# Kernel tuning notes

Hardware: AMD Instinct MI355X
Metric: run time of the kernel (lower is better)

Reference implementation:

```python
import jax, jax.numpy as jnp
import numpy as np

CHANNELS = 32
HIDDEN = 1024
LAYERS = 8
NODE_TYPES = 7
N_NODES = 500_000
N_EDGES = 2_000_000
NUM_GRAPHS = 1024


def setup_inputs() -> dict:
    key = jax.random.key(0)
    ks = jax.random.split(key, 8)
    nodes = jax.random.randint(ks[0], (N_NODES,), 0, NODE_TYPES)
    sources = jax.random.randint(ks[1], (N_EDGES,), 0, N_NODES)
    targets = jax.random.randint(ks[2], (N_EDGES,), 0, N_NODES)
    # sorted graph ids covering all NUM_GRAPHS graphs (no empty graphs)
    batch = (jnp.arange(N_NODES) * NUM_GRAPHS) // N_NODES
    emb = jax.random.normal(ks[3], (NODE_TYPES, CHANNELS), dtype=jnp.float32)
    # xavier-normal-ish init for the 8 layers x {out, back} 32x32 convs
    xavier_std = (2.0 / (CHANNELS + CHANNELS)) ** 0.5
    conv_w = jax.random.normal(ks[4], (LAYERS, 2, CHANNELS, CHANNELS), dtype=jnp.float32) * xavier_std
    hidden_w = jax.random.normal(ks[5], (CHANNELS, HIDDEN), dtype=jnp.float32) * 0.05
    hidden_b = jax.random.normal(ks[6], (HIDDEN,), dtype=jnp.float32) * 0.05
    out_w = jax.random.normal(ks[7], (HIDDEN, 1), dtype=jnp.float32) * 0.05
    return dict(nodes=nodes, sources=sources, targets=targets, batch=batch,
                emb=emb, conv_w=conv_w, hidden_w=hidden_w, hidden_b=hidden_b,
                out_w=out_w)


def reference(nodes, sources, targets, batch, emb, conv_w, hidden_w, hidden_b, out_w):
    n = nodes.shape[0]
    ones_e = jnp.ones(sources.shape[0], dtype=jnp.float32)
    # norm = 1 / (1 + in-degree), norm_t = 1 / (1 + out-degree)  [N,1]
    norm = (1.0 / (1.0 + jax.ops.segment_sum(ones_e, targets, num_segments=n)))[:, None]
    norm_t = (1.0 / (1.0 + jax.ops.segment_sum(ones_e, sources, num_segments=n)))[:, None]
    node_counts = jax.ops.segment_sum(jnp.ones(n, dtype=jnp.float32), batch,
                                      num_segments=NUM_GRAPHS)

    x = emb[nodes]  # [N, C]

    def conv(x, s, t, nrm, w):
        # x.index_add(0, t, x[s]) -> x + scatter_add of gathered source feats
        agg = nrm * (x + jax.ops.segment_sum(x[s], t, num_segments=n))
        return jax.nn.relu(agg @ w)

    for l in range(LAYERS):
        x = x + conv(x, sources, targets, norm, conv_w[l, 0]) \
              + conv(x, targets, sources, norm_t, conv_w[l, 1])

    # mean pooling per graph
    g = jax.ops.segment_sum(x, batch, num_segments=NUM_GRAPHS) / node_counts[:, None]
    h = jax.nn.relu(g @ hidden_w + hidden_b)
    return (h @ out_w).squeeze(-1)  # [NUM_GRAPHS]
```

## Files before the change

### kernel.cpp

```cpp
#include <hip/hip_runtime.h>

#define CHANNELS 32
#define HIDDEN 1024
#define LAYERS 8
#define NRANGE 8

typedef __attribute__((ext_vector_type(8))) short short8;
typedef __attribute__((ext_vector_type(4))) float float4v;

__device__ __forceinline__ short f2bf_rne(float f) {
    union { float f; unsigned u; } v; v.f = f;
    unsigned r = v.u + 0x7fffu + ((v.u >> 16) & 1u);
    return (short)(r >> 16);
}
__device__ __forceinline__ float bf2f(short h) {
    union { float f; unsigned u; } v; v.u = ((unsigned)(unsigned short)h) << 16;
    return v.f;
}
__device__ __forceinline__ float bfu2f(unsigned short h) {
    union { float f; unsigned u; } v; v.u = ((unsigned)h) << 16;
    return v.f;
}
__device__ __forceinline__ float bflo(unsigned u) {
    union { float f; unsigned u; } v; v.u = u << 16; return v.f;
}
__device__ __forceinline__ float bfhi(unsigned u) {
    union { float f; unsigned u; } v; v.u = u & 0xffff0000u; return v.f;
}
__device__ __forceinline__ unsigned packbf(float x, float y) {
    return ((unsigned)(unsigned short)f2bf_rne(y) << 16) |
            (unsigned)(unsigned short)f2bf_rne(x);
}


__global__ __launch_bounds__(256)
void pre_kernel(const int* __restrict__ src, const int* __restrict__ tgt,
                int* __restrict__ deg2,
                const int* __restrict__ nodes, const float* __restrict__ emb,
                unsigned short* __restrict__ hi0, unsigned short* __restrict__ lo,
                const int* __restrict__ batch, float* __restrict__ counts,
                int n_nodes, int n_edges, int n_graphs, int rsh,
                int degB, int initB) {
    int bid = blockIdx.x;
    int tid = threadIdx.x;
    if (bid < degB) {
        int r = bid & (NRANGE - 1);
        int chunk = bid >> 3;
        int base = chunk * 2048;
#pragma unroll
        for (int j = 0; j < 8; j++) {
            int e = base + j * 256 + tid;
            if (e < n_edges) {
                int t = __builtin_nontemporal_load(tgt + e);
                int s = __builtin_nontemporal_load(src + e);
                if ((t >> rsh) == r) atomicAdd(&deg2[t], 1);
                if ((s >> rsh) == r) atomicAdd(&deg2[n_nodes + s], 1);
            }
        }
    } else if (bid < degB + initB) {
        int gid = (bid - degB) * 256 + tid;
        int i = gid >> 2, c8 = (gid & 3) * 8;
        if (i < n_nodes) {
            const float* e = emb + nodes[i] * CHANNELS + c8;
            short8 hv, lv;
#pragma unroll
            for (int k = 0; k < 8; k++) {
                float v = e[k];
                short hsh = f2bf_rne(v);
                hv[k] = hsh;
                lv[k] = f2bf_rne(v - bf2f(hsh));
            }
            *(short8*)(hi0 + (size_t)i * CHANNELS + c8) = hv;
            *(short8*)(lo  + (size_t)i * CHANNELS + c8) = lv;
        }
    } else {
        int b = (bid - degB - initB) * 256 + tid;
        if (b < n_graphs) {
            int lo_i = 0, hi_i = n_nodes;
            while (lo_i < hi_i) { int mid = (lo_i + hi_i) >> 1; if (batch[mid] < b) lo_i = mid + 1; else hi_i = mid; }
            int s0 = lo_i;
            lo_i = 0; hi_i = n_nodes;
            while (lo_i < hi_i) { int mid = (lo_i + hi_i) >> 1; if (batch[mid] < b + 1) lo_i = mid + 1; else hi_i = mid; }
            counts[b] = (float)(lo_i - s0);
        }
    }
}


__global__ __launch_bounds__(256)
void scan_pass1(const int* __restrict__ deg, int* __restrict__ bs, int n) {
    __shared__ int sh[256];
    int t = threadIdx.x;
    int base = blockIdx.x * 2048 + t * 8;
    int s = 0;
#pragma unroll
    for (int j = 0; j < 8; j++) { int idx = base + j; if (idx < n) s += deg[idx]; }
    sh[t] = s; __syncthreads();
    for (int st = 128; st > 0; st >>= 1) { if (t < st) sh[t] += sh[t + st]; __syncthreads(); }
    if (t == 0) bs[blockIdx.x] = sh[0];
}

__global__ void scan_pass2(int* __restrict__ bs, int nb) {
    __shared__ int sh[1024];
    int t = threadIdx.x;
    int v = (t < nb) ? bs[t] : 0;
    sh[t] = v; __syncthreads();
    for (int off = 1; off < 1024; off <<= 1) {
        int u = (t >= off) ? sh[t - off] : 0; __syncthreads();
        sh[t] += u; __syncthreads();
    }
    if (t < nb) bs[t] = sh[t] - v;
}

__global__ __launch_bounds__(256)
void scan_pass3(const int* __restrict__ deg, const int* __restrict__ bs,
                int* __restrict__ off, int* __restrict__ cur, int n) {
    __shared__ int sh[256];
    int t = threadIdx.x;
    int base = blockIdx.x * 2048 + t * 8;
    int v[8]; int s = 0;
#pragma unroll
    for (int j = 0; j < 8; j++) { int idx = base + j; v[j] = (idx < n) ? deg[idx] : 0; s += v[j]; }
    sh[t] = s; __syncthreads();
    for (int st = 1; st < 256; st <<= 1) {
        int u = (t >= st) ? sh[t - st] : 0; __syncthreads();
        sh[t] += u; __syncthreads();
    }
    int acc = bs[blockIdx.x] + sh[t] - s;
#pragma unroll
    for (int j = 0; j < 8; j++) {
        int idx = base + j;
        if (idx < n) { off[idx] = acc; cur[idx] = acc; }
        acc += v[j];
    }
}


__global__ __launch_bounds__(256)
void scatter_range_kernel(const int* __restrict__ src, const int* __restrict__ tgt,
                          int* __restrict__ cur2, int* __restrict__ nbr,
                          int n_nodes, int n_edges, int rsh) {
    int r = blockIdx.x & 15;
    int chunk = blockIdx.x >> 4;
    int base = chunk * 2048;
#pragma unroll
    for (int j = 0; j < 8; j++) {
        int e = base + j * 256 + threadIdx.x;
        if (e < n_edges) {
            int t = __builtin_nontemporal_load(tgt + e);
            int s = __builtin_nontemporal_load(src + e);
            if ((t >> rsh) == r) { int p = atomicAdd(&cur2[t], 1);           nbr[p] = s; }
            if ((s >> rsh) == r) { int q = atomicAdd(&cur2[n_nodes + s], 1); nbr[q] = t; }
        }
    }
}


__global__ __launch_bounds__(256, 8)
void layer_mfma(const int* __restrict__ off2, const int* __restrict__ nbr,
                const float* __restrict__ wbase,
                const unsigned short* __restrict__ hi_in,
                unsigned short* __restrict__ hi_out,
                unsigned short* __restrict__ lo,
                int n_nodes, int n_edges) {
    __shared__ short A1h[64][32], A2h[64][32];
    __shared__ short W0h[32][32], W1h[32][32];
    __shared__ int offIn[65], offOut[65];

    int tid = threadIdx.x;
    int nodeblock = blockIdx.x * 64;

    const unsigned* hid = (const unsigned*)hi_in;
    const unsigned* lod = (const unsigned*)lo;

    for (int idx = tid; idx < CHANNELS * CHANNELS; idx += 256) {
        int k = idx >> 5, n = idx & 31;
        W0h[n][k] = f2bf_rne(wbase[idx]);
        W1h[n][k] = f2bf_rne(wbase[CHANNELS * CHANNELS + idx]);
    }
    if (tid < 65) {
        int idx = nodeblock + tid;
        offIn[tid]  = (idx <= n_nodes) ? off2[idx] : n_edges;
        int idx2 = n_nodes + idx;
        offOut[tid] = (idx2 < 2 * n_nodes) ? off2[idx2] : 2 * n_edges;
    }
    __syncthreads();

    int c = tid & 31, g = tid >> 5;
    int h = c >> 4;
    int cc = c & 15;

    int bi_c, d1_c, bo_c, d2_c, nbl1_c, nbl2_c, node_c;
    float xvx_c, xvy_c;
    {
        int local = g;
        node_c = nodeblock + local;
        bi_c = offIn[local];  d1_c = offIn[local + 1] - bi_c;
        bo_c = offOut[local]; d2_c = offOut[local + 1] - bo_c;
        nbl1_c = (c < d1_c) ? nbr[bi_c + c] : 0;
        nbl2_c = (c < d2_c) ? nbr[bo_c + c] : 0;
        xvx_c = 0.f; xvy_c = 0.f;
        if (node_c < n_nodes) {
            unsigned hp = hid[(unsigned)(node_c * 16 + cc)];
            unsigned lp = lod[(unsigned)(node_c * 16 + cc)];
            xvx_c = bflo(hp) + bflo(lp);
            xvy_c = bfhi(hp) + bfhi(lp);
        }
    }

#define GATHER8(B) { \
    int p0 = __shfl(nbl1_c, (B) + h,     32); \
    int p1 = __shfl(nbl1_c, (B) + 2 + h, 32); \
    int p2 = __shfl(nbl1_c, (B) + 4 + h, 32); \
    int p3 = __shfl(nbl1_c, (B) + 6 + h, 32); \
    int q0 = __shfl(nbl2_c, (B) + h,     32); \
    int q1 = __shfl(nbl2_c, (B) + 2 + h, 32); \
    int q2 = __shfl(nbl2_c, (B) + 4 + h, 32); \
    int q3 = __shfl(nbl2_c, (B) + 6 + h, 32); \
    bool a0 = (B) + h     < m1, a1 = (B) + 2 + h < m1; \
    bool a2 = (B) + 4 + h < m1, a3 = (B) + 6 + h < m1; \
    bool e0 = (B) + h     < m2, e1 = (B) + 2 + h < m2; \
    bool e2 = (B) + 4 + h < m2, e3 = (B) + 6 + h < m2; \
    p0 = a0 ? p0 : self; p1 = a1 ? p1 : self; \
    p2 = a2 ? p2 : self; p3 = a3 ? p3 : self; \
    q0 = e0 ? q0 : self; q1 = e1 ? q1 : self; \
    q2 = e2 ? q2 : self; q3 = e3 ? q3 : self; \
    unsigned u0 = hid[(unsigned)(p0 * 16 + cc)]; \
    unsigned u1 = hid[(unsigned)(p1 * 16 + cc)]; \
    unsigned u2 = hid[(unsigned)(p2 * 16 + cc)]; \
    unsigned u3 = hid[(unsigned)(p3 * 16 + cc)]; \
    unsigned w0 = hid[(unsigned)(q0 * 16 + cc)]; \
    unsigned w1 = hid[(unsigned)(q1 * 16 + cc)]; \
    unsigned w2 = hid[(unsigned)(q2 * 16 + cc)]; \
    unsigned w3 = hid[(unsigned)(q3 * 16 + cc)]; \
    s1x += a0 ? bflo(u0) : 0.f; s1y += a0 ? bfhi(u0) : 0.f; \
    s1x += a1 ? bflo(u1) : 0.f; s1y += a1 ? bfhi(u1) : 0.f; \
    s1x += a2 ? bflo(u2) : 0.f; s1y += a2 ? bfhi(u2) : 0.f; \
    s1x += a3 ? bflo(u3) : 0.f; s1y += a3 ? bfhi(u3) : 0.f; \
    s2x += e0 ? bflo(w0) : 0.f; s2y += e0 ? bfhi(w0) : 0.f; \
    s2x += e1 ? bflo(w1) : 0.f; s2y += e1 ? bfhi(w1) : 0.f; \
    s2x += e2 ? bflo(w2) : 0.f; s2y += e2 ? bfhi(w2) : 0.f; \
    s2x += e3 ? bflo(w3) : 0.f; s2y += e3 ? bfhi(w3) : 0.f; \
}

    for (int pass = 0; pass < 8; pass++) {
        int bi_n = 0, d1_n = 0, bo_n = 0, d2_n = 0, nbl1_n = 0, nbl2_n = 0, node_n = 0;
        float xvx_n = 0.f, xvy_n = 0.f;
        if (pass < 7) {
            int local = (pass + 1) * 8 + g;
            node_n = nodeblock + local;
            bi_n = offIn[local];  d1_n = offIn[local + 1] - bi_n;
            bo_n = offOut[local]; d2_n = offOut[local + 1] - bo_n;
            nbl1_n = (c < d1_n) ? nbr[bi_n + c] : 0;
            nbl2_n = (c < d2_n) ? nbr[bo_n + c] : 0;
            if (node_n < n_nodes) {
                unsigned hp = hid[(unsigned)(node_n * 16 + cc)];
                unsigned lp = lod[(unsigned)(node_n * 16 + cc)];
                xvx_n = bflo(hp) + bflo(lp);
                xvy_n = bfhi(hp) + bfhi(lp);
            }
        }

        int local = pass * 8 + g;
        int i = node_c;
        int self = (i < n_nodes) ? i : 0;

        int m1 = d1_c < 32 ? d1_c : 32;
        int m2 = d2_c < 32 ? d2_c : 32;
        int mm = m1 > m2 ? m1 : m2;

        float s1x = 0.f, s1y = 0.f, s2x = 0.f, s2y = 0.f;
        GATHER8(0)
        if (mm > 8)  GATHER8(8)
        if (mm > 16) GATHER8(16)
        if (mm > 24) GATHER8(24)

        s1x += __shfl_xor(s1x, 16, 32);
        s1y += __shfl_xor(s1y, 16, 32);
        s2x += __shfl_xor(s2x, 16, 32);
        s2y += __shfl_xor(s2y, 16, 32);

        for (int e = bi_c + 32; e < bi_c + d1_c; e++) {
            unsigned u = hid[(unsigned)(nbr[e] * 16 + cc)];
            s1x += bflo(u); s1y += bfhi(u);
        }
        for (int e = bo_c + 32; e < bo_c + d2_c; e++) {
            unsigned u = hid[(unsigned)(nbr[e] * 16 + cc)];
            s2x += bflo(u); s2y += bfhi(u);
        }

        unsigned pk1 = 0, pk2 = 0;
        if (i < n_nodes) {
            float n1 = 1.0f / (1.0f + (float)d1_c);
            float n2 = 1.0f / (1.0f + (float)d2_c);
            pk1 = packbf(n1 * (xvx_c + s1x), n1 * (xvy_c + s1y));
            pk2 = packbf(n2 * (xvx_c + s2x), n2 * (xvy_c + s2y));
        }
        unsigned* dst = (h == 0) ? (unsigned*)&A1h[local][2 * cc]
                                 : (unsigned*)&A2h[local][2 * cc];
        *dst = (h == 0) ? pk1 : pk2;

        bi_c = bi_n; d1_c = d1_n; bo_c = bo_n; d2_c = d2_n;
        nbl1_c = nbl1_n; nbl2_c = nbl2_n;
        xvx_c = xvx_n; xvy_c = xvy_n; node_c = node_n;
    }
#undef GATHER8
    __syncthreads();

    int wv = tid >> 6, lane = tid & 63;
    int m = lane & 15, quad = lane >> 4;
    int row0 = wv * 16;

    short8 a1h = *(const short8*)&A1h[row0 + m][quad * 8];
    short8 a2h = *(const short8*)&A2h[row0 + m][quad * 8];

    float4v dd[4];
#pragma unroll
    for (int hh = 0; hh < 2; hh++) {
        int n0 = hh * 16 + m;
        short8 b0h = *(const short8*)&W0h[n0][quad * 8];
        short8 b1h = *(const short8*)&W1h[n0][quad * 8];
        float4v d1 = {0.f, 0.f, 0.f, 0.f};
        d1 = __builtin_amdgcn_mfma_f32_16x16x32_bf16(a1h, b0h, d1, 0, 0, 0);
        float4v d2 = {0.f, 0.f, 0.f, 0.f};
        d2 = __builtin_amdgcn_mfma_f32_16x16x32_bf16(a2h, b1h, d2, 0, 0, 0);
        dd[hh * 2] = d1; dd[hh * 2 + 1] = d2;
    }

#pragma unroll
    for (int hh = 0; hh < 2; hh++) {
        float4v d1 = dd[hh * 2], d2 = dd[hh * 2 + 1];
#pragma unroll
        for (int r = 0; r < 4; r++) {
            int local = row0 + quad * 4 + r;
            int node = nodeblock + local;
            if (node < n_nodes) {
                int col = hh * 16 + m;
                size_t idx = (size_t)node * CHANNELS + col;
                float base = bfu2f(hi_in[idx]) + bfu2f(lo[idx]);
                float v = base + fmaxf(d1[r], 0.f) + fmaxf(d2[r], 0.f);
                short hn = f2bf_rne(v);
                hi_out[idx] = (unsigned short)hn;
                lo[idx]     = (unsigned short)f2bf_rne(v - bf2f(hn));
            }
        }
    }
}


#define POOL_CHUNK 1024

__global__ __launch_bounds__(256)
void pool_kernel(const int* __restrict__ batch,
                 const unsigned short* __restrict__ hi,
                 const unsigned short* __restrict__ lo,
                 float* __restrict__ g, int n_nodes) {
    int c = threadIdx.x & 31;
    int r = threadIdx.x >> 5;
    int base = blockIdx.x * POOL_CHUNK;
    float acc = 0.f;
    int cur = -1;
    for (int it = 0; it < POOL_CHUNK / 8; it++) {
        int node = base + it * 8 + r;
        if (node >= n_nodes) break;
        int b = batch[node];
        if (b != cur) {
            if (cur >= 0) atomicAdd(&g[cur * CHANNELS + c], acc);
            acc = 0.f;
            cur = b;
        }
        size_t idx = (size_t)node * CHANNELS + c;
        acc += bfu2f(hi[idx]) + bfu2f(lo[idx]);
    }
    if (cur >= 0) atomicAdd(&g[cur * CHANNELS + c], acc);
}


__global__ __launch_bounds__(256)
void mlp_kernel(const float* __restrict__ g, const float* __restrict__ counts,
                const float* __restrict__ hidden_w, const float* __restrict__ hidden_b,
                const float* __restrict__ out_w, float* __restrict__ out) {
    __shared__ float grow[CHANNELS];
    __shared__ float red[256];
    int graph = blockIdx.x;
    int tid = threadIdx.x;
    if (tid < CHANNELS) grow[tid] = g[graph * CHANNELS + tid] / counts[graph];
    __syncthreads();
    float partial = 0.f;
    for (int q = 0; q < HIDDEN / 256; q++) {
        int j = q * 256 + tid;
        float h = hidden_b[j];
#pragma unroll
        for (int k = 0; k < CHANNELS; k++) h += grow[k] * hidden_w[k * HIDDEN + j];
        partial += fmaxf(h, 0.f) * out_w[j];
    }
    red[tid] = partial;
    __syncthreads();
    for (int s = 128; s > 0; s >>= 1) {
        if (tid < s) red[tid] += red[tid + s];
        __syncthreads();
    }
    if (tid == 0) out[graph] = red[0];
}


extern "C" void kernel_launch(void* const* d_in, const int* in_sizes, int n_in,
                              void* d_out, int out_size, void* d_ws, size_t ws_size,
                              hipStream_t stream) {
    const int*   nodes    = (const int*)d_in[0];
    const int*   sources  = (const int*)d_in[1];
    const int*   targets  = (const int*)d_in[2];
    const int*   batch    = (const int*)d_in[3];
    const float* emb      = (const float*)d_in[4];
    const float* conv_w   = (const float*)d_in[5];
    const float* hidden_w = (const float*)d_in[6];
    const float* hidden_b = (const float*)d_in[7];
    const float* out_w    = (const float*)d_in[8];
    float* out = (float*)d_out;

    const int n_nodes  = in_sizes[0];
    const int n_edges  = in_sizes[1];
    const int n_graphs = out_size;
    const int n2 = 2 * n_nodes;

    int rsh8 = 0;
    while (((n_nodes - 1) >> rsh8) >= 8) rsh8++;
    int rsh16 = 0;
    while (((n_nodes - 1) >> rsh16) >= 16) rsh16++;

    char* ws = (char*)d_ws;
    unsigned short* hi0 = (unsigned short*)ws; ws += (size_t)n_nodes * CHANNELS * 2;
    unsigned short* hi1 = (unsigned short*)ws; ws += (size_t)n_nodes * CHANNELS * 2;
    unsigned short* lo  = (unsigned short*)ws; ws += (size_t)n_nodes * CHANNELS * 2;
    int*   deg2   = (int*)ws;   ws += (size_t)n2 * 4;
    int*   off2   = (int*)ws;   ws += (size_t)n2 * 4;
    int*   cur2   = (int*)ws;   ws += (size_t)n2 * 4;
    int*   nbr    = (int*)ws;   ws += (size_t)2 * n_edges * 4;
    int*   bsums  = (int*)ws;   ws += 4096;
    float* g      = (float*)ws; ws += (size_t)n_graphs * CHANNELS * 4;
    float* counts = (float*)ws; ws += (size_t)n_graphs * 4;

    hipMemsetAsync(deg2, 0, (size_t)n2 * 4, stream);
    hipMemsetAsync(g, 0, (size_t)n_graphs * CHANNELS * 4, stream);

    int echunks = (n_edges + 2047) / 2048;
    int degB  = echunks * NRANGE;
    int initB = (n_nodes * 4 + 255) / 256;
    int cntB  = (n_graphs + 255) / 256;

    pre_kernel<<<degB + initB + cntB, 256, 0, stream>>>(sources, targets, deg2,
                                                        nodes, emb, hi0, lo,
                                                        batch, counts,
                                                        n_nodes, n_edges, n_graphs,
                                                        rsh8, degB, initB);

    int nblk = (n2 + 2047) / 2048;
    scan_pass1<<<nblk, 256, 0, stream>>>(deg2, bsums, n2);
    scan_pass2<<<1, 1024, 0, stream>>>(bsums, nblk);
    scan_pass3<<<nblk, 256, 0, stream>>>(deg2, bsums, off2, cur2, n2);

    scatter_range_kernel<<<echunks * 16, 256, 0, stream>>>(sources, targets, cur2, nbr,
                                                           n_nodes, n_edges, rsh16);

    unsigned short* hin = hi0; unsigned short* hout = hi1;
    int lblocks = (n_nodes + 63) / 64;
    for (int l = 0; l < LAYERS; l++) {
        const float* wbase = conv_w + (size_t)l * 2 * CHANNELS * CHANNELS;
        layer_mfma<<<lblocks, 256, 0, stream>>>(off2, nbr, wbase,
                                                hin, hout, lo, n_nodes, n_edges);
        unsigned short* tmp = hin; hin = hout; hout = tmp;
    }

    int pool_blocks = (n_nodes + POOL_CHUNK - 1) / POOL_CHUNK;
    pool_kernel<<<pool_blocks, 256, 0, stream>>>(batch, hin, lo, g, n_nodes);
    mlp_kernel<<<n_graphs, 256, 0, stream>>>(g, counts, hidden_w, hidden_b, out_w, out);
}
```

Measured before the change: 1.560 ms.

## Cache self features in LDS, split gather granularity, adjust launch bounds and pool chunk

Stores each node's reconstructed fp32 self feature in a shared-memory tile during the gather phase, so the epilogue no longer re-reads hi/lo from global memory. The first neighbour gather batch is split into two 4-wide steps so low-degree nodes issue fewer loads. Launch bounds drop from 8 to 4 blocks per SM, and the pooling chunk size doubles. The extra 8 KB of LDS plus the looser occupancy hint may lower resident waves for a latency-bound gather kernel.

```diff
diff --git a/kernel.cpp b/kernel.cpp
--- a/kernel.cpp
+++ b/kernel.cpp
@@ -156,7 +156,7 @@
 }
 
 
-__global__ __launch_bounds__(256, 8)
+__global__ __launch_bounds__(256, 4)
 void layer_mfma(const int* __restrict__ off2, const int* __restrict__ nbr,
                 const float* __restrict__ wbase,
                 const unsigned short* __restrict__ hi_in,
@@ -165,6 +165,7 @@
                 int n_nodes, int n_edges) {
     __shared__ short A1h[64][32], A2h[64][32];
     __shared__ short W0h[32][32], W1h[32][32];
+    __shared__ float Xf[64][32];
     __shared__ int offIn[65], offOut[65];
 
     int tid = threadIdx.x;
@@ -208,40 +209,25 @@
         }
     }
 
-#define GATHER8(B) { \
+#define GATHER4(B) { \
     int p0 = __shfl(nbl1_c, (B) + h,     32); \
     int p1 = __shfl(nbl1_c, (B) + 2 + h, 32); \
-    int p2 = __shfl(nbl1_c, (B) + 4 + h, 32); \
-    int p3 = __shfl(nbl1_c, (B) + 6 + h, 32); \
     int q0 = __shfl(nbl2_c, (B) + h,     32); \
     int q1 = __shfl(nbl2_c, (B) + 2 + h, 32); \
-    int q2 = __shfl(nbl2_c, (B) + 4 + h, 32); \
-    int q3 = __shfl(nbl2_c, (B) + 6 + h, 32); \
     bool a0 = (B) + h     < m1, a1 = (B) + 2 + h < m1; \
-    bool a2 = (B) + 4 + h < m1, a3 = (B) + 6 + h < m1; \
     bool e0 = (B) + h     < m2, e1 = (B) + 2 + h < m2; \
-    bool e2 = (B) + 4 + h < m2, e3 = (B) + 6 + h < m2; \
     p0 = a0 ? p0 : self; p1 = a1 ? p1 : self; \
-    p2 = a2 ? p2 : self; p3 = a3 ? p3 : self; \
     q0 = e0 ? q0 : self; q1 = e1 ? q1 : self; \
-    q2 = e2 ? q2 : self; q3 = e3 ? q3 : self; \
     unsigned u0 = hid[(unsigned)(p0 * 16 + cc)]; \
     unsigned u1 = hid[(unsigned)(p1 * 16 + cc)]; \
-    unsigned u2 = hid[(unsigned)(p2 * 16 + cc)]; \
-    unsigned u3 = hid[(unsigned)(p3 * 16 + cc)]; \
     unsigned w0 = hid[(unsigned)(q0 * 16 + cc)]; \
     unsigned w1 = hid[(unsigned)(q1 * 16 + cc)]; \
-    unsigned w2 = hid[(unsigned)(q2 * 16 + cc)]; \
-    unsigned w3 = hid[(unsigned)(q3 * 16 + cc)]; \
     s1x += a0 ? bflo(u0) : 0.f; s1y += a0 ? bfhi(u0) : 0.f; \
     s1x += a1 ? bflo(u1) : 0.f; s1y += a1 ? bfhi(u1) : 0.f; \
-    s1x += a2 ? bflo(u2) : 0.f; s1y += a2 ? bfhi(u2) : 0.f; \
-    s1x += a3 ? bflo(u3) : 0.f; s1y += a3 ? bfhi(u3) : 0.f; \
     s2x += e0 ? bflo(w0) : 0.f; s2y += e0 ? bfhi(w0) : 0.f; \
     s2x += e1 ? bflo(w1) : 0.f; s2y += e1 ? bfhi(w1) : 0.f; \
-    s2x += e2 ? bflo(w2) : 0.f; s2y += e2 ? bfhi(w2) : 0.f; \
-    s2x += e3 ? bflo(w3) : 0.f; s2y += e3 ? bfhi(w3) : 0.f; \
-}
+}
+#define GATHER8(B) GATHER4(B) GATHER4((B) + 4)
 
     for (int pass = 0; pass < 8; pass++) {
         int bi_n = 0, d1_n = 0, bo_n = 0, d2_n = 0, nbl1_n = 0, nbl2_n = 0, node_n = 0;
@@ -270,7 +256,8 @@
         int mm = m1 > m2 ? m1 : m2;
 
         float s1x = 0.f, s1y = 0.f, s2x = 0.f, s2y = 0.f;
-        GATHER8(0)
+        GATHER4(0)
+        if (mm > 4)  GATHER4(4)
         if (mm > 8)  GATHER8(8)
         if (mm > 16) GATHER8(16)
         if (mm > 24) GATHER8(24)
@@ -299,12 +286,17 @@
         unsigned* dst = (h == 0) ? (unsigned*)&A1h[local][2 * cc]
                                  : (unsigned*)&A2h[local][2 * cc];
         *dst = (h == 0) ? pk1 : pk2;
+        if (h == 0) {
+            Xf[local][2 * cc]     = xvx_c;
+            Xf[local][2 * cc + 1] = xvy_c;
+        }
 
         bi_c = bi_n; d1_c = d1_n; bo_c = bo_n; d2_c = d2_n;
         nbl1_c = nbl1_n; nbl2_c = nbl2_n;
         xvx_c = xvx_n; xvy_c = xvy_n; node_c = node_n;
     }
 #undef GATHER8
+#undef GATHER4
     __syncthreads();
 
     int wv = tid >> 6, lane = tid & 63;
@@ -337,7 +329,7 @@
             if (node < n_nodes) {
                 int col = hh * 16 + m;
                 size_t idx = (size_t)node * CHANNELS + col;
-                float base = bfu2f(hi_in[idx]) + bfu2f(lo[idx]);
+                float base = Xf[local][col];
                 float v = base + fmaxf(d1[r], 0.f) + fmaxf(d2[r], 0.f);
                 short hn = f2bf_rne(v);
                 hi_out[idx] = (unsigned short)hn;
@@ -348,7 +340,7 @@
 }
 
 
-#define POOL_CHUNK 1024
+#define POOL_CHUNK 2048
 
 __global__ __launch_bounds__(256)
 void pool_kernel(const int* __restrict__ batch,
```

Result: slower. 1.939 ms (+24.4%).
